# Kernel tuning notes

Measured on AMD Instinct MI355X. Metric: run time of the kernel, lower is better.

The kernel has to match this reference:

```python
import jax, jax.numpy as jnp
import numpy as np
from math import factorial, sqrt

MUL = 128
LS = (0, 1, 2)
NODE_DIM = MUL * (1 + 3 + 5)   # 1152
N_NODES = 10000
N_EDGES = 50000
EDGE_DIM = 20

# ---------- real Wigner-3j (Clebsch-Gordan) coefficients ----------

def _su2_cg(j1, j2, j3, m1, m2, m3):
    if m1 + m2 != m3:
        return 0.0
    f = lambda n: factorial(int(n))
    pref = sqrt((2 * j3 + 1) * f(j1 + j2 - j3) * f(j1 - j2 + j3) * f(-j1 + j2 + j3) / f(j1 + j2 + j3 + 1))
    pref *= sqrt(f(j3 + m3) * f(j3 - m3) * f(j1 - m1) * f(j1 + m1) * f(j2 - m2) * f(j2 + m2))
    s = 0.0
    for k in range(int(j1 + j2 - j3) + 1):
        if min(j1 - m1 - k, j2 + m2 - k, j3 - j2 + m1 + k, j3 - j1 - m2 + k) < 0:
            continue
        s += (-1) ** k / (f(k) * f(j1 + j2 - j3 - k) * f(j1 - m1 - k) * f(j2 + m2 - k) * f(j3 - j2 + m1 + k) * f(j3 - j1 - m2 + k))
    return pref * s

def _q_real_to_complex(l):
    q = np.zeros((2 * l + 1, 2 * l + 1), dtype=np.complex128)
    for m in range(-l, 0):
        q[l + m, l - m] = 1 / np.sqrt(2)
        q[l + m, l + m] = -1j / np.sqrt(2)
    q[l, l] = 1.0
    for m in range(1, l + 1):
        q[l + m, l + m] = (-1) ** m / np.sqrt(2)
        q[l + m, l - m] = 1j * (-1) ** m / np.sqrt(2)
    return (-1j) ** l * q

def _real_w3j(l1, l2, l3):
    C = np.zeros((2 * l1 + 1, 2 * l2 + 1, 2 * l3 + 1))
    for a in range(2 * l1 + 1):
        for b in range(2 * l2 + 1):
            for c in range(2 * l3 + 1):
                C[a, b, c] = _su2_cg(l1, l2, l3, a - l1, b - l2, c - l3)
    Q1, Q2, Q3 = _q_real_to_complex(l1), _q_real_to_complex(l2), _q_real_to_complex(l3)
    T = np.einsum('abc,ai,bj,ck->ijk', C.astype(np.complex128), Q1, Q2, np.conj(Q3))
    W = T.real if np.linalg.norm(T.real) >= np.linalg.norm(T.imag) else T.imag
    return jnp.asarray(W / np.linalg.norm(W), dtype=jnp.float32)

# instructions from get_feasible_tp(irreps_in, irreps_in, irreps_hidden, 'uuu')
TP_PATHS = [(0, 0, 0), (0, 1, 1), (0, 2, 2), (1, 0, 1), (1, 1, 0), (1, 1, 2),
            (1, 2, 1), (2, 0, 2), (2, 1, 1), (2, 2, 0), (2, 2, 2)]
W3J = {p: _real_w3j(*p) for p in set(TP_PATHS)}
N_PATHS_TO = {0: 3, 1: 4, 2: 4}
PW = {l: float(np.sqrt((2 * l + 1) / N_PATHS_TO[l])) for l in LS}  # e3nn component/element norm
WEIGHT_NUMEL = len(TP_PATHS) * MUL  # 1408

# ---------- irreps helpers (e3nn layout: per-irrep [mul, 2l+1] blocks) ----------

def split_irreps(x):
    n = x.shape[0]
    s = x[:, :MUL]
    v1 = x[:, MUL:4 * MUL].reshape(n, MUL, 3)
    v2 = x[:, 4 * MUL:].reshape(n, MUL, 5)
    return s, v1, v2

def merge_irreps(s, v1, v2):
    n = s.shape[0]
    return jnp.concatenate([s, v1.reshape(n, -1), v2.reshape(n, -1)], axis=-1)

def o3_linear(x, W0, W1, W2, b0=None):
    s, v1, v2 = split_irreps(x)
    inv = 1.0 / np.sqrt(MUL)  # e3nn fan-in normalization
    s = s @ W0 * inv + (b0 if b0 is not None else 0.0)
    v1 = jnp.einsum('num,uv->nvm', v1, W1) * inv
    v2 = jnp.einsum('num,uv->nvm', v2, W2) * inv
    return merge_irreps(s, v1, v2)

def norm_gate(x, W1, b1, W2, b2):
    s, v1, v2 = split_irreps(x)
    n1 = jnp.linalg.norm(v1, axis=-1)  # [N, 128]
    n2 = jnp.linalg.norm(v2, axis=-1)
    f0 = jnp.concatenate([s, n1, n2], axis=-1)  # [N, 384]
    g = jax.nn.silu(f0 @ W1 + b1) @ W2 + b2
    return merge_irreps(g[:, :MUL], v1 * g[:, MUL:2 * MUL, None], v2 * g[:, 2 * MUL:, None])

def equiv_dot(x1, x2):
    s1, v11, v21 = split_irreps(x1)
    s2, v12, v22 = split_irreps(x2)
    d0 = s1 * s2
    d1 = jnp.sum(v11 * v12, -1) / np.sqrt(3.0)
    d2 = jnp.sum(v21 * v22, -1) / np.sqrt(5.0)
    return jnp.concatenate([d0, d1, d2], -1)  # [E, 384]

def tp_node_pair(x1, x2, weights):
    s1, v11, v21 = split_irreps(x1)
    s2, v12, v22 = split_irreps(x2)
    parts1 = [s1[:, :, None], v11, v21]
    parts2 = [s2[:, :, None], v12, v22]
    outs = {l: 0.0 for l in LS}
    for p, (l1, l2, l3) in enumerate(TP_PATHS):
        w = weights[:, p * MUL:(p + 1) * MUL]  # [E, 128]
        outs[l3] = outs[l3] + PW[l3] * jnp.einsum(
            'eui,euj,ijk,eu->euk', parts1[l1], parts2[l2], W3J[(l1, l2, l3)], w)
    return merge_irreps(outs[0][:, :, 0], outs[1], outs[2])

# ---------- inputs ----------

def setup_inputs() -> dict:
    key = jax.random.key(0)
    ks = jax.random.split(key, 30)
    lin = lambda k, fi, fo: jax.random.normal(k, (fi, fo), jnp.float32) / np.sqrt(fi)
    vec = lambda k, d: jax.random.normal(k, (d,), jnp.float32) * 0.1
    NI = 3 * MUL  # 384 = num_irreps
    return {
        'x': jax.random.normal(ks[0], (N_NODES, NODE_DIM), jnp.float32),
        'edge_attr': jax.random.uniform(ks[1], (N_EDGES, EDGE_DIM), jnp.float32),
        'edge_index': jax.random.randint(ks[2], (2, N_EDGES), 0, N_NODES, jnp.int32),
        'W_pre0': jax.random.normal(ks[3], (MUL, MUL), jnp.float32),
        'W_pre1': jax.random.normal(ks[4], (MUL, MUL), jnp.float32),
        'W_pre2': jax.random.normal(ks[5], (MUL, MUL), jnp.float32),
        'b_pre0': vec(ks[6], MUL),
        'ngpre_W1': lin(ks[7], NI, NI), 'ngpre_b1': vec(ks[8], NI),
        'ngpre_W2': lin(ks[9], NI, NI), 'ngpre_b2': vec(ks[10], NI),
        'es_W1': lin(ks[11], MUL + NI, 128), 'es_b1': vec(ks[12], 128),
        'es_W2': lin(ks[13], 128, WEIGHT_NUMEL), 'es_b2': vec(ks[14], WEIGHT_NUMEL),
        'er_W1': lin(ks[15], EDGE_DIM, 128), 'er_b1': vec(ks[16], 128),
        'er_W2': lin(ks[17], 128, WEIGHT_NUMEL), 'er_b2': vec(ks[18], WEIGHT_NUMEL),
        'ngpost_W1': lin(ks[19], NI, NI), 'ngpost_b1': vec(ks[20], NI),
        'ngpost_W2': lin(ks[21], NI, NI), 'ngpost_b2': vec(ks[22], NI),
        'W_post0': jax.random.normal(ks[23], (MUL, MUL), jnp.float32),
        'W_post1': jax.random.normal(ks[24], (MUL, MUL), jnp.float32),
        'W_post2': jax.random.normal(ks[25], (MUL, MUL), jnp.float32),
    }

def reference(x, edge_attr, edge_index,
              W_pre0, W_pre1, W_pre2, b_pre0,
              ngpre_W1, ngpre_b1, ngpre_W2, ngpre_b2,
              es_W1, es_b1, es_W2, es_b2,
              er_W1, er_b1, er_W2, er_b2,
              ngpost_W1, ngpost_b1, ngpost_W2, ngpost_b2,
              W_post0, W_post1, W_post2):
    src, dst = edge_index[0], edge_index[1]
    xs, xd = x[src], x[dst]
    dots = equiv_dot(xs, xd)[:, MUL:]  # drop 0e dots: [E, 256]
    s0 = jnp.concatenate([xs[:, :MUL], xd[:, :MUL], dots], axis=-1)  # [E, 512]
    tp_w = (jax.nn.silu(s0 @ es_W1 + es_b1) @ es_W2 + es_b2) \
         * (jax.nn.silu(edge_attr @ er_W1 + er_b1) @ er_W2 + er_b2)  # [E, 1408]
    x_prime = norm_gate(o3_linear(x, W_pre0, W_pre1, W_pre2, b_pre0),
                        ngpre_W1, ngpre_b1, ngpre_W2, ngpre_b2)
    fij = tp_node_pair(x_prime[src], x_prime[dst], tp_w)  # [E, 1152]
    fij = norm_gate(fij, ngpost_W1, ngpost_b1, ngpost_W2, ngpost_b2)
    fij = o3_linear(fij, W_post0, W_post1, W_post2)
    return fij
```

## Files before the change

kernel.cpp:

```cpp
#include <hip/hip_runtime.h>
#include <math.h>

#define NNODES 10000
#define NEDGES 50000
#define ND 1152
#define MUL 128
#define WNW 1408
#define EDIM 20

#define CK1 0.5773502691896258f
#define CK2 0.4472135954999579f
#define A2C 0.31622776601683794f
#define A0A (-0.18257418583505536f)
#define A0B 0.3651483716701107f
#define B1C 0.11952286093343936f
#define B2C 0.23904572186687873f
#define B3C 0.20701966780270626f
#define PW0 0.5773502691896258f
#define PW1 0.8660254037844386f
#define PW2 1.1180339887498949f
#define INV128 0.08838834764831845f

__device__ __forceinline__ float silu_f(float v) { return v / (1.f + expf(-v)); }

typedef short bfrag __attribute__((ext_vector_type(8)));
typedef float f32x4 __attribute__((ext_vector_type(4)));

__device__ __forceinline__ ushort f2bf(float f) {
    uint u = __float_as_uint(f);
    u += 0x7fffu + ((u >> 16) & 1u);
    return (ushort)(u >> 16);
}
__device__ __forceinline__ float bf2f(ushort h) {
    return __uint_as_float(((uint)h) << 16);
}

#define LSTR 40

template<bool DUAL, bool SILU>
__global__ __launch_bounds__(256) void gemmbf(
    const float* __restrict__ A1, int lda,
    const ushort* __restrict__ B1H, const ushort* __restrict__ B1L,
    const float* __restrict__ b1,
    const float* __restrict__ A2,
    const ushort* __restrict__ B2H, const ushort* __restrict__ B2L,
    const float* __restrict__ b2,
    float* __restrict__ C, int ldc, int M, int K)
{
    __shared__ __align__(16) ushort Ah[128 * LSTR];
    __shared__ __align__(16) ushort Al[128 * LSTR];
    __shared__ __align__(16) ushort Bh[128 * LSTR];
    __shared__ __align__(16) ushort Bl[128 * LSTR];

    const int tid = threadIdx.x;
    const int l   = tid & 63;
    const int wid = tid >> 6;
    const int wr  = (wid >> 1) << 6;
    const int wc  = (wid & 1) << 6;
    const int rowBase = blockIdx.y << 7;
    const int n0      = blockIdx.x << 7;

    const int sRow = tid >> 1;
    const int sK   = (tid & 1) << 4;
    const int bN   = tid & 127;
    const int bK   = (tid >> 7) << 4;

    const int frow = l & 15;
    const int fk   = (l >> 4) << 3;

    f32x4 acc0[4][4], acc1[4][4];
#pragma unroll
    for (int m = 0; m < 4; ++m)
#pragma unroll
        for (int n = 0; n < 4; ++n) {
            acc0[m][n] = f32x4{0.f, 0.f, 0.f, 0.f};
            if constexpr (DUAL) acc1[m][n] = f32x4{0.f, 0.f, 0.f, 0.f};
        }

#pragma unroll
    for (int ph = 0; ph < (DUAL ? 2 : 1); ++ph) {
        const float*  A  = (DUAL && ph) ? A2  : A1;
        const ushort* BH = (DUAL && ph) ? B2H : B1H;
        const ushort* BL = (DUAL && ph) ? B2L : B1L;
        for (int k0 = 0; k0 < K; k0 += 32) {
            float f[16];
            int grow = rowBase + sRow;
            if (grow < M) {
                const float4* p = (const float4*)&A[(size_t)grow * lda + k0 + sK];
#pragma unroll
                for (int j = 0; j < 4; ++j) {
                    float4 v = p[j];
                    f[j * 4 + 0] = v.x; f[j * 4 + 1] = v.y;
                    f[j * 4 + 2] = v.z; f[j * 4 + 3] = v.w;
                }
            } else {
#pragma unroll
                for (int j = 0; j < 16; ++j) f[j] = 0.f;
            }
            {
                int base = sRow * LSTR + sK;
#pragma unroll
                for (int j = 0; j < 4; ++j) {
                    ushort4 hv, lv;
                    hv.x = f2bf(f[j * 4 + 0]); lv.x = f2bf(f[j * 4 + 0] - bf2f(hv.x));
                    hv.y = f2bf(f[j * 4 + 1]); lv.y = f2bf(f[j * 4 + 1] - bf2f(hv.y));
                    hv.z = f2bf(f[j * 4 + 2]); lv.z = f2bf(f[j * 4 + 2] - bf2f(hv.z));
                    hv.w = f2bf(f[j * 4 + 3]); lv.w = f2bf(f[j * 4 + 3] - bf2f(hv.w));
                    *(ushort4*)&Ah[base + j * 4] = hv;
                    *(ushort4*)&Al[base + j * 4] = lv;
                }
            }
            {
                size_t go = (size_t)(n0 + bN) * K + k0 + bK;
                uint4 h0 = *(const uint4*)&BH[go];
                uint4 h1 = *(const uint4*)&BH[go + 8];
                uint4 l0 = *(const uint4*)&BL[go];
                uint4 l1 = *(const uint4*)&BL[go + 8];
                int bb = bN * LSTR + bK;
                *(uint4*)&Bh[bb]     = h0;
                *(uint4*)&Bh[bb + 8] = h1;
                *(uint4*)&Bl[bb]     = l0;
                *(uint4*)&Bl[bb + 8] = l1;
            }
            __syncthreads();
            bfrag bhF[4], blF[4];
#pragma unroll
            for (int n = 0; n < 4; ++n) {
                int r = (wc + n * 16 + frow) * LSTR + fk;
                bhF[n] = *(const bfrag*)&Bh[r];
                blF[n] = *(const bfrag*)&Bl[r];
            }
#pragma unroll
            for (int m = 0; m < 4; ++m) {
                int r = (wr + m * 16 + frow) * LSTR + fk;
                bfrag ah = *(const bfrag*)&Ah[r];
                bfrag al = *(const bfrag*)&Al[r];
#pragma unroll
                for (int n = 0; n < 4; ++n) {
                    f32x4 a = (DUAL && ph) ? acc1[m][n] : acc0[m][n];
                    a = __builtin_amdgcn_mfma_f32_16x16x32_bf16(ah, bhF[n], a, 0, 0, 0);
                    a = __builtin_amdgcn_mfma_f32_16x16x32_bf16(ah, blF[n], a, 0, 0, 0);
                    a = __builtin_amdgcn_mfma_f32_16x16x32_bf16(al, bhF[n], a, 0, 0, 0);
                    if (DUAL && ph) acc1[m][n] = a; else acc0[m][n] = a;
                }
            }
            __syncthreads();
        }
    }

#pragma unroll
    for (int n = 0; n < 4; ++n) {
        int col = n0 + wc + n * 16 + frow;
        float bb1 = b1[col];
        float bb2 = DUAL ? b2[col] : 0.f;
#pragma unroll
        for (int m = 0; m < 4; ++m) {
            int row0 = rowBase + wr + m * 16 + ((l >> 4) << 2);
#pragma unroll
            for (int q = 0; q < 4; ++q) {
                int row = row0 + q;
                if (row >= M) continue;
                float v;
                if constexpr (DUAL) {
                    v = (acc0[m][n][q] + bb1) * (acc1[m][n][q] + bb2);
                } else {
                    v = acc0[m][n][q] + bb1;
                    if constexpr (SILU) v = silu_f(v);
                }
                C[(size_t)row * ldc + col] = v;
            }
        }
    }
}

template<int NPL, int OFF, int GOFF>
__global__ __launch_bounds__(256) void o3postbf(
    const float* __restrict__ fij, size_t FP,
    const float* __restrict__ g,
    const ushort* __restrict__ WH, const ushort* __restrict__ WL,
    float* __restrict__ out, int M)
{
    __shared__ __align__(16) ushort Ah[NPL * 32 * LSTR];
    __shared__ __align__(16) ushort Al[NPL * 32 * LSTR];
    __shared__ __align__(16) ushort Bh[128 * LSTR];
// ... 84 lines not shown
    for (int n = 0; n < 4; ++n) {
        int col = wc + n * 16 + frow;
#pragma unroll
        for (int q = 0; q < 4; ++q) {
            int row = rowBase + wr + ((l >> 4) << 2) + q;
            if (row >= M) continue;
            float* po = &out[(size_t)row * ND + OFF + col * NPL];
#pragma unroll
            for (int p = 0; p < NPL; ++p)
                po[p] = acc[p][n][q] * INV128;
        }
    }
}

__global__ void wsplit_kernel(
    const float* __restrict__ W0, const float* __restrict__ W1,
    const float* __restrict__ W2, const float* __restrict__ W3,
    const float* __restrict__ W4, const float* __restrict__ W5,
    const float* __restrict__ W6, const float* __restrict__ W7,
    const float* __restrict__ W8,
    ushort* __restrict__ out)
{
    int m = blockIdx.y;
    const float* W; int K, N; size_t off;
    switch (m) {
        case 0:  W = W0; K = 128; N = 1408; off = 0;        break;
        case 1:  W = W1; K = 128; N = 1408; off = 360448;   break;
        case 2:  W = W2; K = 384; N = 384;  off = 720896;   break;
        case 3:  W = W3; K = 384; N = 384;  off = 1015808;  break;
        case 4:  W = W4; K = 384; N = 384;  off = 1310720;  break;
        case 5:  W = W5; K = 384; N = 384;  off = 1605632;  break;
        case 6:  W = W6; K = 128; N = 128;  off = 1900544;  break;
        case 7:  W = W7; K = 128; N = 128;  off = 1933312;  break;
        default: W = W8; K = 128; N = 128;  off = 1966080;  break;
    }
    int idx = blockIdx.x * 256 + threadIdx.x;
    if (idx >= K * N) return;
    int k = idx / N, n = idx - k * N;
    float v = W[idx];
    ushort h  = f2bf(v);
    ushort lo = f2bf(v - bf2f(h));
    size_t KN = (size_t)K * N;
    out[off + (size_t)n * K + k]      = h;
    out[off + KN + (size_t)n * K + k] = lo;
}

template<int AMODE, int OMODE, bool SILU, bool FMUL, bool O3S>
__global__ __launch_bounds__(256) void gemm128(
    const float* __restrict__ A, int lda,
    const float* __restrict__ B, int ldb,
    const float* __restrict__ W1p, const float* __restrict__ W2p,
    const float* __restrict__ bias, const float* __restrict__ M2,
    float* __restrict__ C, int ldc, int M, int K,
    const float* __restrict__ xg, const int* __restrict__ ei,
    const float* __restrict__ dots)
{
    __shared__ float Ast[32][132];
    __shared__ float Bs[32][132];

    const int tid = threadIdx.x;
    const int tx = tid & 15, ty = tid >> 4;
    const int rowBase = blockIdx.y << 7;
    const int n0 = blockIdx.x << 7;
    const int z = blockIdx.z;

    int off = 0, stride = 1;
    if constexpr (AMODE == 2 || AMODE == 3 || AMODE == 4 || OMODE == 1 || O3S) {
        if (z == 0)      { off = 0;             stride = 1; }
        else if (z < 4)  { off = 128 + (z - 1); stride = 3; }
        else             { off = 512 + (z - 4); stride = 5; }
    }
    const float* Bz = B;
    if constexpr (AMODE >= 2) {
        if (z >= 1 && z < 4) Bz = W1p;
        else if (z >= 4)     Bz = W2p;
    }
    const float* Ab = A;
    if constexpr (AMODE == 3 || AMODE == 4) Ab = A + (size_t)z * M * lda;
    float* Cb = C;
    if constexpr (OMODE == 2) Cb = C + (size_t)z * M * ldc;

    float acc[2][2][4][4] = {};

    for (int k0 = 0; k0 < K; k0 += 32) {
#pragma unroll
        for (int i = 0; i < 4; ++i) {
            int f4 = tid + (i << 8);
            int row = f4 >> 3;
            int kq  = (f4 & 7) << 2;
            int grow = rowBase + row, gk = k0 + kq;
            float4 v = make_float4(0.f, 0.f, 0.f, 0.f);
            if (grow < M) {
                if constexpr (AMODE == 0 || AMODE == 3) {
                    if (gk + 4 <= K) {
                        v = *(const float4*)&Ab[(size_t)grow * lda + gk];
                    } else {
                        float t[4] = {0.f, 0.f, 0.f, 0.f};
#pragma unroll
                        for (int j = 0; j < 4; ++j)
                            if (gk + j < K) t[j] = Ab[(size_t)grow * lda + gk + j];
                        v = make_float4(t[0], t[1], t[2], t[3]);
                    }
                } else if constexpr (AMODE == 1) {
                    if (gk < 128)
                        v = *(const float4*)&xg[(size_t)ei[grow] * ND + gk];
                    else if (gk < 256)
                        v = *(const float4*)&xg[(size_t)ei[NEDGES + grow] * ND + (gk - 128)];
                    else
                        v = *(const float4*)&dots[(size_t)grow * 256 + (gk - 256)];
                } else if constexpr (AMODE == 2) {
                    const float* p = &Ab[(size_t)grow * ND + off];
                    v.x = p[(gk + 0) * stride];
                    v.y = p[(gk + 1) * stride];
                    v.z = p[(gk + 2) * stride];
                    v.w = p[(gk + 3) * stride];
                } else {
                    int gsel = (z == 0) ? 0 : (z < 4 ? 128 : 256);
                    float4 vg = *(const float4*)&xg[(size_t)grow * 384 + gsel + gk];
                    if (z == 0) {
                        v = vg;
                    } else {
                        float4 vf = *(const float4*)&Ab[(size_t)grow * lda + gk];
                        v = make_float4(vf.x * vg.x, vf.y * vg.y,
                                        vf.z * vg.z, vf.w * vg.w);
                    }
                }
            }
            Ast[kq + 0][row] = v.x;
            Ast[kq + 1][row] = v.y;
            Ast[kq + 2][row] = v.z;
            Ast[kq + 3][row] = v.w;
        }
#pragma unroll
        for (int i = 0; i < 4; ++i) {
            int f4 = tid + (i << 8);
            int bk = f4 >> 5;
            int nq = (f4 & 31) << 2;
            float4 v = make_float4(0.f, 0.f, 0.f, 0.f);
            if (k0 + bk < K)
                v = *(const float4*)&Bz[(size_t)(k0 + bk) * ldb + n0 + nq];
            *(float4*)&Bs[bk][nq] = v;
        }
        __syncthreads();
#pragma unroll
        for (int kk = 0; kk < 32; ++kk) {
            float4 a0 = *(const float4*)&Ast[kk][(ty << 2)];
            float4 a1 = *(const float4*)&Ast[kk][64 + (ty << 2)];
            float4 b0 = *(const float4*)&Bs[kk][(tx << 2)];
            float4 b1 = *(const float4*)&Bs[kk][64 + (tx << 2)];
            float ar[2][4] = {{a0.x, a0.y, a0.z, a0.w}, {a1.x, a1.y, a1.z, a1.w}};
            float br[2][4] = {{b0.x, b0.y, b0.z, b0.w}, {b1.x, b1.y, b1.z, b1.w}};
#pragma unroll
            for (int h = 0; h < 2; ++h)
#pragma unroll
                for (int g = 0; g < 2; ++g)
#pragma unroll
                    for (int ii = 0; ii < 4; ++ii)
#pragma unroll
                        for (int jj = 0; jj < 4; ++jj)
                            acc[h][g][ii][jj] = fmaf(ar[h][ii], br[g][jj], acc[h][g][ii][jj]);
        }
        __syncthreads();
    }

#pragma unroll
    for (int h = 0; h < 2; ++h) {
#pragma unroll
        for (int ii = 0; ii < 4; ++ii) {
            int row = rowBase + (h << 6) + (ty << 2) + ii;
            if (row >= M) continue;
#pragma unroll
            for (int g = 0; g < 2; ++g) {
                int colq = n0 + (g << 6) + (tx << 2);
                float o[4];
#pragma unroll
                for (int jj = 0; jj < 4; ++jj) {
                    float v = acc[h][g][ii][jj];
                    int col = colq + jj;
                    if constexpr (O3S) {
                        v *= INV128;
                        if (bias && z == 0) v += bias[col];
                    } else {
                        if (bias) v += bias[col];
                    }
                    if constexpr (SILU) v = silu_f(v);
                    if constexpr (FMUL) v *= M2[(size_t)row * ldc + col];
                    o[jj] = v;
                }
                if constexpr (OMODE == 1) {
                    float* p = &Cb[(size_t)row * ND + off];
#pragma unroll
                    for (int jj = 0; jj < 4; ++jj) p[(colq + jj) * stride] = o[jj];
                } else {
                    *(float4*)&Cb[(size_t)row * ldc + colq] =
                        make_float4(o[0], o[1], o[2], o[3]);
                }
            }
        }
    }
}

__global__ void dots_kernel(const float* __restrict__ x, const int* __restrict__ ei,
                            float* __restrict__ dots)
{
    int idx = blockIdx.x * 256 + threadIdx.x;
    int e = idx >> 8, t = idx & 255;
    if (e >= NEDGES) return;
    const float* ps = x + (size_t)ei[e] * ND;
    const float* pd = x + (size_t)ei[NEDGES + e] * ND;
    float v;
    if (t < 128) {
        int u = 128 + t * 3;
        v = (ps[u] * pd[u] + ps[u + 1] * pd[u + 1] + ps[u + 2] * pd[u + 2]) * CK1;
    } else {
        int u = 512 + (t - 128) * 5;
        v = (ps[u] * pd[u] + ps[u + 1] * pd[u + 1] + ps[u + 2] * pd[u + 2]
             + ps[u + 3] * pd[u + 3] + ps[u + 4] * pd[u + 4]) * CK2;
    }
    dots[idx] = v;
}

__global__ void f0_kernel(const float* __restrict__ in, float* __restrict__ f0, int M)
{
    int idx = blockIdx.x * 256 + threadIdx.x;
    int r = idx / 384, t = idx - r * 384;
    if (r >= M) return;
    size_t P = (size_t)M * 128;
    const float* p = in + (size_t)r * 128;
    float v;
    if (t < 128) v = p[t];
    else if (t < 256) {
        int u = t - 128;
        float x1 = p[P + u], x2 = p[2 * P + u], x3 = p[3 * P + u];
        v = sqrtf(x1 * x1 + x2 * x2 + x3 * x3);
    } else {
        int u = t - 256;
        float x1 = p[4 * P + u], x2 = p[5 * P + u], x3 = p[6 * P + u],
              x4 = p[7 * P + u], x5 = p[8 * P + u];
        v = sqrtf(x1 * x1 + x2 * x2 + x3 * x3 + x4 * x4 + x5 * x5);
    }
    f0[(size_t)r * 384 + t] = v;
}

__global__ void gate_kernel(float* __restrict__ xp, const float* __restrict__ g, int M)
{
    int t = blockIdx.x * 256 + threadIdx.x;
    if (t >= M * 128) return;
    int z = blockIdx.y;
    int r = t >> 7, u = t & 127;
    float* p = xp + (size_t)z * M * 128 + t;
    const float* gr = g + (size_t)r * 384;
    if (z == 0)      *p = gr[u];
    else if (z < 4)  *p *= gr[128 + u];
    else             *p *= gr[256 + u];
}

__global__ __launch_bounds__(256) void tp_kernel(
    const float* __restrict__ xp, const int* __restrict__ ei,
    const float* __restrict__ tpw, float* __restrict__ fij,
    float* __restrict__ f0, int e0, int ec)
{
    int le = blockIdx.x * 2 + (threadIdx.x >> 7);
    int u = threadIdx.x & 127;
    if (le >= ec) return;
    int e = e0 + le;
    const size_t NP = (size_t)NNODES * 128;
    const float* ps = xp + (size_t)ei[e] * 128 + u;
    const float* pd = xp + (size_t)ei[NEDGES + e] * 128 + u;

    float ss = ps[0], sd = pd[0];
    float a0 = ps[NP],     a1 = ps[2 * NP], a2 = ps[3 * NP];
    float b0 = pd[NP],     b1 = pd[2 * NP], b2 = pd[3 * NP];
    float c0 = ps[4 * NP], c1 = ps[5 * NP], c2 = ps[6 * NP],
          c3 = ps[7 * NP], c4 = ps[8 * NP];
    float d0 = pd[4 * NP], d1 = pd[5 * NP], d2 = pd[6 * NP],
// ... 35 lines not shown
    float o2_1 = PW2 * (CK2 * (w2 * ss * d1 + w7 * c1 * sd) + w5 * S1 + w10 * V1);
    float o2_2 = PW2 * (CK2 * (w2 * ss * d2 + w7 * c2 * sd) + w5 * S2 + w10 * V2);
    float o2_3 = PW2 * (CK2 * (w2 * ss * d3 + w7 * c3 * sd) + w5 * S3 + w10 * V3);
    float o2_4 = PW2 * (CK2 * (w2 * ss * d4 + w7 * c4 * sd) + w5 * S4 + w10 * V4);

    size_t FP = (size_t)ec * 128;
    float* po = fij + (size_t)le * 128 + u;
    po[0] = o_s;
    po[FP] = o1_0;     po[2 * FP] = o1_1; po[3 * FP] = o1_2;
    po[4 * FP] = o2_0; po[5 * FP] = o2_1; po[6 * FP] = o2_2;
    po[7 * FP] = o2_3; po[8 * FP] = o2_4;

    float n1 = sqrtf(o1_0 * o1_0 + o1_1 * o1_1 + o1_2 * o1_2);
    float n2 = sqrtf(o2_0 * o2_0 + o2_1 * o2_1 + o2_2 * o2_2
                     + o2_3 * o2_3 + o2_4 * o2_4);
    float* pf = f0 + (size_t)le * 384;
    pf[u] = o_s;
    pf[128 + u] = n1;
    pf[256 + u] = n2;
}

extern "C" void kernel_launch(void* const* d_in, const int* in_sizes, int n_in,
                              void* d_out, int out_size, void* d_ws, size_t ws_size,
                              hipStream_t stream)
{
    const float* x         = (const float*)d_in[0];
    const float* edge_attr = (const float*)d_in[1];
    const int*   ei        = (const int*)  d_in[2];
    const float* W_pre0    = (const float*)d_in[3];
    const float* W_pre1    = (const float*)d_in[4];
    const float* W_pre2    = (const float*)d_in[5];
    const float* b_pre0    = (const float*)d_in[6];
    const float* ngpre_W1  = (const float*)d_in[7];
    const float* ngpre_b1  = (const float*)d_in[8];
// ... 6 lines not shown
    const float* er_W1     = (const float*)d_in[15];
    const float* er_b1     = (const float*)d_in[16];
    const float* er_W2     = (const float*)d_in[17];
    const float* er_b2     = (const float*)d_in[18];
    const float* ngpost_W1 = (const float*)d_in[19];
    const float* ngpost_b1 = (const float*)d_in[20];
    const float* ngpost_W2 = (const float*)d_in[21];
    const float* ngpost_b2 = (const float*)d_in[22];
    const float* W_post0   = (const float*)d_in[23];
    const float* W_post1   = (const float*)d_in[24];
    const float* W_post2   = (const float*)d_in[25];
    float* out = (float*)d_out;
    float* ws  = (float*)d_ws;

    float* xp    = ws;
    float* hes   = ws + (size_t)9 * NNODES * 128;
    float* her   = hes + (size_t)NEDGES * 128;
    ushort* wsp  = (ushort*)(her + (size_t)NEDGES * 128);
    const ushort* esW2tH   = wsp;
    const ushort* esW2tL   = wsp + 180224;
    const ushort* erW2tH   = wsp + 360448;
    const ushort* erW2tL   = wsp + 540672;
    const ushort* preW1H   = wsp + 720896;
    const ushort* preW1L   = wsp + 868352;
    const ushort* preW2H   = wsp + 1015808;
    const ushort* preW2L   = wsp + 1163264;
    const ushort* postW1H  = wsp + 1310720;
    const ushort* postW1L  = wsp + 1458176;
    const ushort* postW2H  = wsp + 1605632;
    const ushort* postW2L  = wsp + 1753088;
    const ushort* o3pW0H   = wsp + 1900544;
    const ushort* o3pW0L   = wsp + 1916928;
    const ushort* o3pW1H   = wsp + 1933312;
    const ushort* o3pW1L   = wsp + 1949696;
    const ushort* o3pW2H   = wsp + 1966080;
    const ushort* o3pW2L   = wsp + 1982464;
    float* arena = her + (size_t)NEDGES * 128 + 999424;

    long ws_floats = (long)(ws_size / 4);
    long arena_f = ws_floats - 25319424L;
    long ec0 = arena_f / 2944;
    if (ec0 > NEDGES) ec0 = NEDGES;
    if (ec0 < 1) ec0 = 1;
    int NC = (int)((NEDGES + ec0 - 1) / ec0);
    int Ec = (NEDGES + NC - 1) / NC;

    float* dots = arena;

    wsplit_kernel<<<dim3(704, 9), 256, 0, stream>>>(
        es_W2, er_W2, ngpre_W1, ngpre_W2, ngpost_W1, ngpost_W2,
        W_post0, W_post1, W_post2, wsp);

    dots_kernel<<<NEDGES, 256, 0, stream>>>(x, ei, dots);

    dim3 gE(1, (NEDGES + 127) / 128);
    gemm128<1, 0, true, false, false><<<gE, 256, 0, stream>>>(
        nullptr, 0, es_W1, 128, nullptr, nullptr, es_b1, nullptr,
        hes, 128, NEDGES, 512, x, ei, dots);
    gemm128<0, 0, true, false, false><<<gE, 256, 0, stream>>>(
        edge_attr, EDIM, er_W1, 128, nullptr, nullptr, er_b1, nullptr,
        her, 128, NEDGES, EDIM, nullptr, nullptr, nullptr);

    dim3 gO3p(1, (NNODES + 127) / 128, 9);
    gemm128<2, 2, false, false, true><<<gO3p, 256, 0, stream>>>(
        x, 0, W_pre0, 128, W_pre1, W_pre2, b_pre0, nullptr,
        xp, 128, NNODES, 128, nullptr, nullptr, nullptr);

    float* f0n = arena;
    float* hb  = f0n + (size_t)NNODES * 384;
    float* gb  = hb + (size_t)NNODES * 384;
    f0_kernel<<<((size_t)NNODES * 384 + 255) / 256, 256, 0, stream>>>(xp, f0n, NNODES);
    dim3 gNGp(3, (NNODES + 127) / 128);
    gemmbf<false, true><<<gNGp, 256, 0, stream>>>(
        f0n, 384, preW1H, preW1L, ngpre_b1,
        nullptr, nullptr, nullptr, nullptr,
        hb, 384, NNODES, 384);
    gemmbf<false, false><<<gNGp, 256, 0, stream>>>(
        hb, 384, preW2H, preW2L, ngpre_b2,
        nullptr, nullptr, nullptr, nullptr,
        gb, 384, NNODES, 384);
    dim3 gGp((NNODES * 128 + 255) / 256, 9);
    gate_kernel<<<gGp, 256, 0, stream>>>(xp, gb, NNODES);

    for (int c = 0; c < NC; ++c) {
        int e0 = c * Ec;
        int ec = NEDGES - e0; if (ec > Ec) ec = Ec;
        if (ec <= 0) break;

        float* tpwc = arena;
        float* fijc = tpwc + (size_t)Ec * 1408;
        float* f0p  = fijc + (size_t)Ec * 1152;

        dim3 gW(11, (ec + 127) / 128);
        gemmbf<true, false><<<gW, 256, 0, stream>>>(
            hes + (size_t)e0 * 128, 128, esW2tH, esW2tL, es_b2,
            her + (size_t)e0 * 128, erW2tH, erW2tL, er_b2,
            tpwc, WNW, ec, 128);

        tp_kernel<<<(ec + 1) / 2, 256, 0, stream>>>(xp, ei, tpwc, fijc, f0p, e0, ec);

        float* h1p = tpwc;
        float* gp  = tpwc + (size_t)Ec * 384;
        dim3 gNG(3, (ec + 127) / 128);
        gemmbf<false, true><<<gNG, 256, 0, stream>>>(
            f0p, 384, postW1H, postW1L, ngpost_b1,
            nullptr, nullptr, nullptr, nullptr,
            h1p, 384, ec, 384);
        gemmbf<false, false><<<gNG, 256, 0, stream>>>(
            h1p, 384, postW2H, postW2L, ngpost_b2,
            nullptr, nullptr, nullptr, nullptr,
            gp, 384, ec, 384);

        size_t FPc = (size_t)ec * 128;
        int nb = (ec + 31) / 32;
        o3postbf<1, 0, 0><<<nb, 256, 0, stream>>>(
            nullptr, 0, gp, o3pW0H, o3pW0L, out + (size_t)e0 * ND, ec);
        o3postbf<3, 128, 128><<<nb, 256, 0, stream>>>(
            fijc + FPc, FPc, gp, o3pW1H, o3pW1L, out + (size_t)e0 * ND, ec);
        o3postbf<5, 512, 256><<<nb, 256, 0, stream>>>(
            fijc + 4 * FPc, FPc, gp, o3pW2H, o3pW2L, out + (size_t)e0 * ND, ec);
    }
}
```

Baseline: 1.414 ms.

## Move remaining fp32 GEMMs to split-bf16 MFMA and store intermediates pre-split

The scalar fp32 gemm128 kernel is replaced by the split-bf16 MFMA gemmbf kernel for the edge-MLP first layers and the pre o3_linear, using new gather and strided input modes. Intermediate activations (hes, her, f0, hidden layers) are now written as hi/lo bf16 pairs, so consumers load them directly instead of converting fp32 in every tile. The aim is to replace FMA-bound scalar GEMMs with matrix-core work and to halve intermediate traffic. The cost is more template variants, element-wise strided or unvectorized loads in the edge_attr and o3 paths, and a changed workspace layout.

```diff
diff --git a/kernel.cpp b/kernel.cpp
--- a/kernel.cpp
+++ b/kernel.cpp
@@ -37,15 +37,19 @@
 
 #define LSTR 40
 
-template<bool DUAL, bool SILU>
+template<int DUAL, int SILU, int ASRC, int OSINK>
 __global__ __launch_bounds__(256) void gemmbf(
-    const float* __restrict__ A1, int lda,
+    const void* __restrict__ A1p, const void* __restrict__ A1s, int lda,
     const ushort* __restrict__ B1H, const ushort* __restrict__ B1L,
     const float* __restrict__ b1,
-    const float* __restrict__ A2,
+    const void* __restrict__ A2p, const void* __restrict__ A2s,
     const ushort* __restrict__ B2H, const ushort* __restrict__ B2L,
     const float* __restrict__ b2,
-    float* __restrict__ C, int ldc, int M, int K)
+    const ushort* __restrict__ W2H, const ushort* __restrict__ W2L,
+    float* __restrict__ C, ushort* __restrict__ CH, ushort* __restrict__ CL,
+    int ldc, int M, int K, int Kreal,
+    const float* __restrict__ xg, const int* __restrict__ ei,
+    const float* __restrict__ dots)
 {
     __shared__ __align__(16) ushort Ah[128 * LSTR];
     __shared__ __align__(16) ushort Al[128 * LSTR];
@@ -68,6 +72,14 @@
     const int frow = l & 15;
     const int fk   = (l >> 4) << 3;
 
+    const int z = (ASRC == 3) ? blockIdx.z : 0;
+    int zoff = 0, zstride = 1;
+    if constexpr (ASRC == 3) {
+        if (z == 0)      { zoff = 0;             zstride = 1; }
+        else if (z < 4)  { zoff = 128 + (z - 1); zstride = 3; }
+        else             { zoff = 512 + (z - 4); zstride = 5; }
+    }
+
     f32x4 acc0[4][4], acc1[4][4];
 #pragma unroll
     for (int m = 0; m < 4; ++m)
@@ -79,48 +91,89 @@
 
 #pragma unroll
     for (int ph = 0; ph < (DUAL ? 2 : 1); ++ph) {
-        const float*  A  = (DUAL && ph) ? A2  : A1;
+        const void* Ap  = (DUAL && ph) ? A2p : A1p;
+        const void* Asp = (DUAL && ph) ? A2s : A1s;
         const ushort* BH = (DUAL && ph) ? B2H : B1H;
         const ushort* BL = (DUAL && ph) ? B2L : B1L;
+        if constexpr (ASRC == 3) {
+            if (z >= 1 && z < 4) { BH = B2H; BL = B2L; }
+            else if (z >= 4)     { BH = W2H; BL = W2L; }
+        }
+
         for (int k0 = 0; k0 < K; k0 += 32) {
-            float f[16];
-            int grow = rowBase + sRow;
-            if (grow < M) {
-                const float4* p = (const float4*)&A[(size_t)grow * lda + k0 + sK];
-#pragma unroll
-                for (int j = 0; j < 4; ++j) {
-                    float4 v = p[j];
-                    f[j * 4 + 0] = v.x; f[j * 4 + 1] = v.y;
-                    f[j * 4 + 2] = v.z; f[j * 4 + 3] = v.w;
-                }
-            } else {
-#pragma unroll
-                for (int j = 0; j < 16; ++j) f[j] = 0.f;
-            }
             {
-                int base = sRow * LSTR + sK;
-#pragma unroll
-                for (int j = 0; j < 4; ++j) {
-                    ushort4 hv, lv;
-                    hv.x = f2bf(f[j * 4 + 0]); lv.x = f2bf(f[j * 4 + 0] - bf2f(hv.x));
-                    hv.y = f2bf(f[j * 4 + 1]); lv.y = f2bf(f[j * 4 + 1] - bf2f(hv.y));
-                    hv.z = f2bf(f[j * 4 + 2]); lv.z = f2bf(f[j * 4 + 2] - bf2f(hv.z));
-                    hv.w = f2bf(f[j * 4 + 3]); lv.w = f2bf(f[j * 4 + 3] - bf2f(hv.w));
-                    *(ushort4*)&Ah[base + j * 4] = hv;
-                    *(ushort4*)&Al[base + j * 4] = lv;
+                int grow = rowBase + sRow;
+                if constexpr (ASRC == 1) {
+                    uint4 h0 = {0,0,0,0}, h1v = {0,0,0,0};
+                    uint4 l0 = {0,0,0,0}, l1v = {0,0,0,0};
+                    if (grow < M) {
+                        const ushort* AH = ((const ushort*)Ap)  + (size_t)grow * lda + k0 + sK;
+                        const ushort* AL = ((const ushort*)Asp) + (size_t)grow * lda + k0 + sK;
+                        h0  = *(const uint4*)AH; h1v = *(const uint4*)(AH + 8);
+                        l0  = *(const uint4*)AL; l1v = *(const uint4*)(AL + 8);
+                    }
+                    int base = sRow * LSTR + sK;
+                    *(uint4*)&Ah[base]     = h0;  *(uint4*)&Ah[base + 8] = h1v;
+                    *(uint4*)&Al[base]     = l0;  *(uint4*)&Al[base + 8] = l1v;
+                } else {
+                    float f[16];
+                    if (grow < M) {
+                        if constexpr (ASRC == 0) {
+#pragma unroll
+                            for (int j = 0; j < 16; ++j) {
+                                int gk = k0 + sK + j;
+                                f[j] = (gk < Kreal)
+                                     ? ((const float*)Ap)[(size_t)grow * lda + gk] : 0.f;
+                            }
+                        } else if constexpr (ASRC == 2) {
+                            int gk = k0 + sK;
+                            const float4* p;
+                            if (gk < 128)
+                                p = (const float4*)&xg[(size_t)ei[grow] * ND + gk];
+                            else if (gk < 256)
+                                p = (const float4*)&xg[(size_t)ei[NEDGES + grow] * ND + (gk - 128)];
+                            else
+                                p = (const float4*)&dots[(size_t)grow * 256 + (gk - 256)];
+#pragma unroll
+                            for (int j = 0; j < 4; ++j) {
+                                float4 v = p[j];
+                                f[j*4+0] = v.x; f[j*4+1] = v.y;
+                                f[j*4+2] = v.z; f[j*4+3] = v.w;
+                            }
+                        } else {
+                            const float* p = &((const float*)Ap)[(size_t)grow * lda + zoff];
+#pragma unroll
+                            for (int j = 0; j < 16; ++j)
+                                f[j] = p[(k0 + sK + j) * zstride];
+                        }
+                    } else {
+#pragma unroll
+                        for (int j = 0; j < 16; ++j) f[j] = 0.f;
+                    }
+                    int base = sRow * LSTR + sK;
+#pragma unroll
+                    for (int j = 0; j < 4; ++j) {
+                        ushort4 hv, lv;
+                        hv.x = f2bf(f[j*4+0]); lv.x = f2bf(f[j*4+0] - bf2f(hv.x));
+                        hv.y = f2bf(f[j*4+1]); lv.y = f2bf(f[j*4+1] - bf2f(hv.y));
+                        hv.z = f2bf(f[j*4+2]); lv.z = f2bf(f[j*4+2] - bf2f(hv.z));
+                        hv.w = f2bf(f[j*4+3]); lv.w = f2bf(f[j*4+3] - bf2f(hv.w));
+                        *(ushort4*)&Ah[base + j*4] = hv;
+                        *(ushort4*)&Al[base + j*4] = lv;
+                    }
                 }
             }
             {
                 size_t go = (size_t)(n0 + bN) * K + k0 + bK;
                 uint4 h0 = *(const uint4*)&BH[go];
-                uint4 h1 = *(const uint4*)&BH[go + 8];
+                uint4 h1v = *(const uint4*)&BH[go + 8];
                 uint4 l0 = *(const uint4*)&BL[go];
-                uint4 l1 = *(const uint4*)&BL[go + 8];
+                uint4 l1v = *(const uint4*)&BL[go + 8];
                 int bb = bN * LSTR + bK;
                 *(uint4*)&Bh[bb]     = h0;
-                *(uint4*)&Bh[bb + 8] = h1;
+                *(uint4*)&Bh[bb + 8] = h1v;
                 *(uint4*)&Bl[bb]     = l0;
-                *(uint4*)&Bl[bb + 8] = l1;
+                *(uint4*)&Bl[bb + 8] = l1v;
             }
             __syncthreads();
             bfrag bhF[4], blF[4];
@@ -151,8 +204,8 @@
 #pragma unroll
     for (int n = 0; n < 4; ++n) {
         int col = n0 + wc + n * 16 + frow;
-        float bb1 = b1[col];
-        float bb2 = DUAL ? b2[col] : 0.f;
+        float bb1 = b1 ? b1[col] : 0.f;
+        float bb2 = (DUAL && b2) ? b2[col] : 0.f;
 #pragma unroll
         for (int m = 0; m < 4; ++m) {
             int row0 = rowBase + wr + m * 16 + ((l >> 4) << 2);
@@ -160,14 +213,25 @@
             for (int q = 0; q < 4; ++q) {
                 int row = row0 + q;
                 if (row >= M) continue;
-                float v;
                 if constexpr (DUAL) {
-                    v = (acc0[m][n][q] + bb1) * (acc1[m][n][q] + bb2);
+                    float v = (acc0[m][n][q] + bb1) * (acc1[m][n][q] + bb2);
+                    C[(size_t)row * ldc + col] = v;
+                } else if constexpr (OSINK == 0) {
+                    float v = acc0[m][n][q] + bb1;
+                    if constexpr (SILU) v = silu_f(v);
+                    C[(size_t)row * ldc + col] = v;
+                } else if constexpr (OSINK == 1) {
+                    float v = acc0[m][n][q] + bb1;
+                    if constexpr (SILU) v = silu_f(v);
+                    ushort h  = f2bf(v);
+                    ushort lo = f2bf(v - bf2f(h));
+                    CH[(size_t)row * ldc + col] = h;
+                    CL[(size_t)row * ldc + col] = lo;
                 } else {
-                    v = acc0[m][n][q] + bb1;
-                    if constexpr (SILU) v = silu_f(v);
+                    float v = acc0[m][n][q] * INV128;
+                    if (z == 0 && b1) v += b1[col];
+                    C[(size_t)z * M * ldc + (size_t)row * ldc + col] = v;
                 }
-                C[(size_t)row * ldc + col] = v;
             }
         }
     }
@@ -282,190 +346,42 @@
 }
 
 __global__ void wsplit_kernel(
-    const float* __restrict__ W0, const float* __restrict__ W1,
-    const float* __restrict__ W2, const float* __restrict__ W3,
-    const float* __restrict__ W4, const float* __restrict__ W5,
-    const float* __restrict__ W6, const float* __restrict__ W7,
-    const float* __restrict__ W8,
+    const float* __restrict__ W0,  const float* __restrict__ W1,
+    const float* __restrict__ W2,  const float* __restrict__ W3,
+    const float* __restrict__ W4,  const float* __restrict__ W5,
+    const float* __restrict__ W6,  const float* __restrict__ W7,
+    const float* __restrict__ W8,  const float* __restrict__ W9,
+    const float* __restrict__ W10, const float* __restrict__ W11,
+    const float* __restrict__ W12, const float* __restrict__ W13,
     ushort* __restrict__ out)
 {
     int m = blockIdx.y;
-    const float* W; int K, N; size_t off;
+    const float* W; int K, Kp, N; size_t off;
     switch (m) {
-        case 0:  W = W0; K = 128; N = 1408; off = 0;        break;
-        case 1:  W = W1; K = 128; N = 1408; off = 360448;   break;
-        case 2:  W = W2; K = 384; N = 384;  off = 720896;   break;
-        case 3:  W = W3; K = 384; N = 384;  off = 1015808;  break;
-        case 4:  W = W4; K = 384; N = 384;  off = 1310720;  break;
-        case 5:  W = W5; K = 384; N = 384;  off = 1605632;  break;
-        case 6:  W = W6; K = 128; N = 128;  off = 1900544;  break;
-        case 7:  W = W7; K = 128; N = 128;  off = 1933312;  break;
-        default: W = W8; K = 128; N = 128;  off = 1966080;  break;
+        case 0:  W = W0;  K = 128; Kp = 128; N = 1408; off = 0;       break;
+        case 1:  W = W1;  K = 128; Kp = 128; N = 1408; off = 360448;  break;
+        case 2:  W = W2;  K = 384; Kp = 384; N = 384;  off = 720896;  break;
+        case 3:  W = W3;  K = 384; Kp = 384; N = 384;  off = 1015808; break;
+        case 4:  W = W4;  K = 384; Kp = 384; N = 384;  off = 1310720; break;
+        case 5:  W = W5;  K = 384; Kp = 384; N = 384;  off = 1605632; break;
+        case 6:  W = W6;  K = 128; Kp = 128; N = 128;  off = 1900544; break;
+        case 7:  W = W7;  K = 128; Kp = 128; N = 128;  off = 1933312; break;
+        case 8:  W = W8;  K = 128; Kp = 128; N = 128;  off = 1966080; break;
+        case 9:  W = W9;  K = 128; Kp = 128; N = 128;  off = 1998848; break;
+        case 10: W = W10; K = 128; Kp = 128; N = 128;  off = 2031616; break;
+        case 11: W = W11; K = 128; Kp = 128; N = 128;  off = 2064384; break;
+        case 12: W = W12; K = 512; Kp = 512; N = 128;  off = 2097152; break;
+        default: W = W13; K = 20;  Kp = 32;  N = 128;  off = 2228224; break;
     }
     int idx = blockIdx.x * 256 + threadIdx.x;
-    if (idx >= K * N) return;
+    if (idx >= Kp * N) return;
     int k = idx / N, n = idx - k * N;
-    float v = W[idx];
+    float v = (k < K) ? W[(size_t)k * N + n] : 0.f;
     ushort h  = f2bf(v);
     ushort lo = f2bf(v - bf2f(h));
-    size_t KN = (size_t)K * N;
-    out[off + (size_t)n * K + k]      = h;
-    out[off + KN + (size_t)n * K + k] = lo;
-}
-
-template<int AMODE, int OMODE, bool SILU, bool FMUL, bool O3S>
-__global__ __launch_bounds__(256) void gemm128(
-    const float* __restrict__ A, int lda,
-    const float* __restrict__ B, int ldb,
-    const float* __restrict__ W1p, const float* __restrict__ W2p,
-    const float* __restrict__ bias, const float* __restrict__ M2,
-    float* __restrict__ C, int ldc, int M, int K,
-    const float* __restrict__ xg, const int* __restrict__ ei,
-    const float* __restrict__ dots)
-{
-    __shared__ float Ast[32][132];
-    __shared__ float Bs[32][132];
-
-    const int tid = threadIdx.x;
-    const int tx = tid & 15, ty = tid >> 4;
-    const int rowBase = blockIdx.y << 7;
-    const int n0 = blockIdx.x << 7;
-    const int z = blockIdx.z;
-
-    int off = 0, stride = 1;
-    if constexpr (AMODE == 2 || AMODE == 3 || AMODE == 4 || OMODE == 1 || O3S) {
-        if (z == 0)      { off = 0;             stride = 1; }
-        else if (z < 4)  { off = 128 + (z - 1); stride = 3; }
-        else             { off = 512 + (z - 4); stride = 5; }
-    }
-    const float* Bz = B;
-    if constexpr (AMODE >= 2) {
-        if (z >= 1 && z < 4) Bz = W1p;
-        else if (z >= 4)     Bz = W2p;
-    }
-    const float* Ab = A;
-    if constexpr (AMODE == 3 || AMODE == 4) Ab = A + (size_t)z * M * lda;
-    float* Cb = C;
-    if constexpr (OMODE == 2) Cb = C + (size_t)z * M * ldc;
-
-    float acc[2][2][4][4] = {};
-
-    for (int k0 = 0; k0 < K; k0 += 32) {
-#pragma unroll
-        for (int i = 0; i < 4; ++i) {
-            int f4 = tid + (i << 8);
-            int row = f4 >> 3;
-            int kq  = (f4 & 7) << 2;
-            int grow = rowBase + row, gk = k0 + kq;
-            float4 v = make_float4(0.f, 0.f, 0.f, 0.f);
-            if (grow < M) {
-                if constexpr (AMODE == 0 || AMODE == 3) {
-                    if (gk + 4 <= K) {
-                        v = *(const float4*)&Ab[(size_t)grow * lda + gk];
-                    } else {
-                        float t[4] = {0.f, 0.f, 0.f, 0.f};
-#pragma unroll
-                        for (int j = 0; j < 4; ++j)
-                            if (gk + j < K) t[j] = Ab[(size_t)grow * lda + gk + j];
-                        v = make_float4(t[0], t[1], t[2], t[3]);
-                    }
-                } else if constexpr (AMODE == 1) {
-                    if (gk < 128)
-                        v = *(const float4*)&xg[(size_t)ei[grow] * ND + gk];
-                    else if (gk < 256)
-                        v = *(const float4*)&xg[(size_t)ei[NEDGES + grow] * ND + (gk - 128)];
-                    else
-                        v = *(const float4*)&dots[(size_t)grow * 256 + (gk - 256)];
-                } else if constexpr (AMODE == 2) {
-                    const float* p = &Ab[(size_t)grow * ND + off];
-                    v.x = p[(gk + 0) * stride];
-                    v.y = p[(gk + 1) * stride];
-                    v.z = p[(gk + 2) * stride];
-                    v.w = p[(gk + 3) * stride];
-                } else {
-                    int gsel = (z == 0) ? 0 : (z < 4 ? 128 : 256);
-                    float4 vg = *(const float4*)&xg[(size_t)grow * 384 + gsel + gk];
-                    if (z == 0) {
-                        v = vg;
-                    } else {
-                        float4 vf = *(const float4*)&Ab[(size_t)grow * lda + gk];
-                        v = make_float4(vf.x * vg.x, vf.y * vg.y,
-                                        vf.z * vg.z, vf.w * vg.w);
-                    }
-                }
-            }
-            Ast[kq + 0][row] = v.x;
-            Ast[kq + 1][row] = v.y;
-            Ast[kq + 2][row] = v.z;
-            Ast[kq + 3][row] = v.w;
-        }
-#pragma unroll
-        for (int i = 0; i < 4; ++i) {
-            int f4 = tid + (i << 8);
-            int bk = f4 >> 5;
-            int nq = (f4 & 31) << 2;
-            float4 v = make_float4(0.f, 0.f, 0.f, 0.f);
-            if (k0 + bk < K)
-                v = *(const float4*)&Bz[(size_t)(k0 + bk) * ldb + n0 + nq];
-            *(float4*)&Bs[bk][nq] = v;
-        }
-        __syncthreads();
-#pragma unroll
-        for (int kk = 0; kk < 32; ++kk) {
-            float4 a0 = *(const float4*)&Ast[kk][(ty << 2)];
-            float4 a1 = *(const float4*)&Ast[kk][64 + (ty << 2)];
-            float4 b0 = *(const float4*)&Bs[kk][(tx << 2)];
-            float4 b1 = *(const float4*)&Bs[kk][64 + (tx << 2)];
-            float ar[2][4] = {{a0.x, a0.y, a0.z, a0.w}, {a1.x, a1.y, a1.z, a1.w}};
-            float br[2][4] = {{b0.x, b0.y, b0.z, b0.w}, {b1.x, b1.y, b1.z, b1.w}};
-#pragma unroll
-            for (int h = 0; h < 2; ++h)
-#pragma unroll
-                for (int g = 0; g < 2; ++g)
-#pragma unroll
-                    for (int ii = 0; ii < 4; ++ii)
-#pragma unroll
-                        for (int jj = 0; jj < 4; ++jj)
-                            acc[h][g][ii][jj] = fmaf(ar[h][ii], br[g][jj], acc[h][g][ii][jj]);
-        }
-        __syncthreads();
-    }
-
-#pragma unroll
-    for (int h = 0; h < 2; ++h) {
-#pragma unroll
-        for (int ii = 0; ii < 4; ++ii) {
-            int row = rowBase + (h << 6) + (ty << 2) + ii;
-            if (row >= M) continue;
-#pragma unroll
-            for (int g = 0; g < 2; ++g) {
-                int colq = n0 + (g << 6) + (tx << 2);
-                float o[4];
-#pragma unroll
-                for (int jj = 0; jj < 4; ++jj) {
-                    float v = acc[h][g][ii][jj];
-                    int col = colq + jj;
-                    if constexpr (O3S) {
-                        v *= INV128;
-                        if (bias && z == 0) v += bias[col];
-                    } else {
-                        if (bias) v += bias[col];
-                    }
-                    if constexpr (SILU) v = silu_f(v);
-                    if constexpr (FMUL) v *= M2[(size_t)row * ldc + col];
-                    o[jj] = v;
-                }
-                if constexpr (OMODE == 1) {
-                    float* p = &Cb[(size_t)row * ND + off];
-#pragma unroll
-                    for (int jj = 0; jj < 4; ++jj) p[(colq + jj) * stride] = o[jj];
-                } else {
-                    *(float4*)&Cb[(size_t)row * ldc + colq] =
-                        make_float4(o[0], o[1], o[2], o[3]);
-                }
-            }
-        }
-    }
+    size_t KN = (size_t)Kp * N;
+    out[off + (size_t)n * Kp + k]      = h;
+    out[off + KN + (size_t)n * Kp + k] = lo;
 }
 
 __global__ void dots_kernel(const float* __restrict__ x, const int* __restrict__ ei,
@@ -488,7 +404,8 @@
     dots[idx] = v;
 }
 
-__global__ void f0_kernel(const float* __restrict__ in, float* __restrict__ f0, int M)
+__global__ void f0_kernel(const float* __restrict__ in,
+                          ushort* __restrict__ f0H, ushort* __restrict__ f0L, int M)
 {
     int idx = blockIdx.x * 256 + threadIdx.x;
     int r = idx / 384, t = idx - r * 384;
@@ -507,7 +424,9 @@
               x4 = p[7 * P + u], x5 = p[8 * P + u];
         v = sqrtf(x1 * x1 + x2 * x2 + x3 * x3 + x4 * x4 + x5 * x5);
     }
-    f0[(size_t)r * 384 + t] = v;
+    ushort h = f2bf(v);
+    f0H[(size_t)r * 384 + t] = h;
+    f0L[(size_t)r * 384 + t] = f2bf(v - bf2f(h));
 }
 
 __global__ void gate_kernel(float* __restrict__ xp, const float* __restrict__ g, int M)
@@ -526,7 +445,7 @@
 __global__ __launch_bounds__(256) void tp_kernel(
     const float* __restrict__ xp, const int* __restrict__ ei,
     const float* __restrict__ tpw, float* __restrict__ fij,
-    float* __restrict__ f0, int e0, int ec)
+    ushort* __restrict__ f0H, ushort* __restrict__ f0L, int e0, int ec)
 {
     int le = blockIdx.x * 2 + (threadIdx.x >> 7);
     int u = threadIdx.x & 127;
@@ -592,10 +511,11 @@
     float n1 = sqrtf(o1_0 * o1_0 + o1_1 * o1_1 + o1_2 * o1_2);
     float n2 = sqrtf(o2_0 * o2_0 + o2_1 * o2_1 + o2_2 * o2_2
                      + o2_3 * o2_3 + o2_4 * o2_4);
-    float* pf = f0 + (size_t)le * 384;
-    pf[u] = o_s;
-    pf[128 + u] = n1;
-    pf[256 + u] = n2;
+    size_t fb = (size_t)le * 384;
+    ushort h;
+    h = f2bf(o_s); f0H[fb + u]       = h; f0L[fb + u]       = f2bf(o_s - bf2f(h));
+    h = f2bf(n1);  f0H[fb + 128 + u] = h; f0L[fb + 128 + u] = f2bf(n1 - bf2f(h));
+    h = f2bf(n2);  f0H[fb + 256 + u] = h; f0L[fb + 256 + u] = f2bf(n2 - bf2f(h));
 }
 
 extern "C" void kernel_launch(void* const* d_in, const int* in_sizes, int n_in,
@@ -632,31 +552,43 @@
     float* ws  = (float*)d_ws;
 
     float* xp    = ws;
-    float* hes   = ws + (size_t)9 * NNODES * 128;
-    float* her   = hes + (size_t)NEDGES * 128;
-    ushort* wsp  = (ushort*)(her + (size_t)NEDGES * 128);
-    const ushort* esW2tH   = wsp;
-    const ushort* esW2tL   = wsp + 180224;
-    const ushort* erW2tH   = wsp + 360448;
-    const ushort* erW2tL   = wsp + 540672;
-    const ushort* preW1H   = wsp + 720896;
-    const ushort* preW1L   = wsp + 868352;
-    const ushort* preW2H   = wsp + 1015808;
-    const ushort* preW2L   = wsp + 1163264;
-    const ushort* postW1H  = wsp + 1310720;
-    const ushort* postW1L  = wsp + 1458176;
-    const ushort* postW2H  = wsp + 1605632;
-    const ushort* postW2L  = wsp + 1753088;
-    const ushort* o3pW0H   = wsp + 1900544;
-    const ushort* o3pW0L   = wsp + 1916928;
-    const ushort* o3pW1H   = wsp + 1933312;
-    const ushort* o3pW1L   = wsp + 1949696;
-    const ushort* o3pW2H   = wsp + 1966080;
-    const ushort* o3pW2L   = wsp + 1982464;
-    float* arena = her + (size_t)NEDGES * 128 + 999424;
+    ushort* hesH = (ushort*)ws + 23040000;
+    ushort* hesL = hesH + 6400000;
+    ushort* herH = hesL + 6400000;
+    ushort* herL = herH + 6400000;
+    ushort* wsp  = herL + 6400000;
+    const ushort* esW2H  = wsp;
+    const ushort* esW2L  = wsp + 180224;
+    const ushort* erW2H  = wsp + 360448;
+    const ushort* erW2L  = wsp + 540672;
+    const ushort* preW1H = wsp + 720896;
+    const ushort* preW1L = wsp + 868352;
+    const ushort* preW2H = wsp + 1015808;
+    const ushort* preW2L = wsp + 1163264;
+    const ushort* postW1H = wsp + 1310720;
+    const ushort* postW1L = wsp + 1458176;
+    const ushort* postW2H = wsp + 1605632;
+    const ushort* postW2L = wsp + 1753088;
+    const ushort* o3pW0H = wsp + 1900544;
+    const ushort* o3pW0L = wsp + 1916928;
+    const ushort* o3pW1H = wsp + 1933312;
+    const ushort* o3pW1L = wsp + 1949696;
+    const ushort* o3pW2H = wsp + 1966080;
+    const ushort* o3pW2L = wsp + 1982464;
+    const ushort* preL0H = wsp + 1998848;
+    const ushort* preL0L = wsp + 2015232;
+    const ushort* preL1H = wsp + 2031616;
+    const ushort* preL1L = wsp + 2048000;
+    const ushort* preL2H = wsp + 2064384;
+    const ushort* preL2L = wsp + 2080768;
+    const ushort* esW1H  = wsp + 2097152;
+    const ushort* esW1L  = wsp + 2162688;
+    const ushort* erW1H  = wsp + 2228224;
+    const ushort* erW1L  = wsp + 2232320;
+    float* arena = ws + 25438208;
 
     long ws_floats = (long)(ws_size / 4);
-    long arena_f = ws_floats - 25319424L;
+    long arena_f = ws_floats - 25438208L;
     long ec0 = arena_f / 2944;
     if (ec0 > NEDGES) ec0 = NEDGES;
     if (ec0 < 1) ec0 = 1;
@@ -665,38 +597,44 @@
 
     float* dots = arena;
 
-    wsplit_kernel<<<dim3(704, 9), 256, 0, stream>>>(
+    wsplit_kernel<<<dim3(704, 14), 256, 0, stream>>>(
         es_W2, er_W2, ngpre_W1, ngpre_W2, ngpost_W1, ngpost_W2,
-        W_post0, W_post1, W_post2, wsp);
+        W_post0, W_post1, W_post2, W_pre0, W_pre1, W_pre2,
+        es_W1, er_W1, wsp);
 
     dots_kernel<<<NEDGES, 256, 0, stream>>>(x, ei, dots);
 
     dim3 gE(1, (NEDGES + 127) / 128);
-    gemm128<1, 0, true, false, false><<<gE, 256, 0, stream>>>(
-        nullptr, 0, es_W1, 128, nullptr, nullptr, es_b1, nullptr,
-        hes, 128, NEDGES, 512, x, ei, dots);
-    gemm128<0, 0, true, false, false><<<gE, 256, 0, stream>>>(
-        edge_attr, EDIM, er_W1, 128, nullptr, nullptr, er_b1, nullptr,
-        her, 128, NEDGES, EDIM, nullptr, nullptr, nullptr);
+    gemmbf<0, 1, 2, 1><<<gE, 256, 0, stream>>>(
+        nullptr, nullptr, 0, esW1H, esW1L, es_b1,
+        nullptr, nullptr, nullptr, nullptr, nullptr, nullptr, nullptr,
+        nullptr, hesH, hesL, 128, NEDGES, 512, 512, x, ei, dots);
+    gemmbf<0, 1, 0, 1><<<gE, 256, 0, stream>>>(
+        edge_attr, nullptr, EDIM, erW1H, erW1L, er_b1,
+        nullptr, nullptr, nullptr, nullptr, nullptr, nullptr, nullptr,
+        nullptr, herH, herL, 128, NEDGES, 32, EDIM, nullptr, nullptr, nullptr);
 
     dim3 gO3p(1, (NNODES + 127) / 128, 9);
-    gemm128<2, 2, false, false, true><<<gO3p, 256, 0, stream>>>(
-        x, 0, W_pre0, 128, W_pre1, W_pre2, b_pre0, nullptr,
-        xp, 128, NNODES, 128, nullptr, nullptr, nullptr);
-
-    float* f0n = arena;
-    float* hb  = f0n + (size_t)NNODES * 384;
-    float* gb  = hb + (size_t)NNODES * 384;
-    f0_kernel<<<((size_t)NNODES * 384 + 255) / 256, 256, 0, stream>>>(xp, f0n, NNODES);
+    gemmbf<0, 0, 3, 2><<<gO3p, 256, 0, stream>>>(
+        x, nullptr, ND, preL0H, preL0L, b_pre0,
+        nullptr, nullptr, preL1H, preL1L, nullptr, preL2H, preL2L,
+        xp, nullptr, nullptr, 128, NNODES, 128, 128, nullptr, nullptr, nullptr);
+
+    ushort* f0nH = (ushort*)arena;
+    ushort* f0nL = f0nH + (size_t)NNODES * 384;
+    ushort* hbH  = f0nL + (size_t)NNODES * 384;
+    ushort* hbL  = hbH + (size_t)NNODES * 384;
+    float*  gb   = arena + (size_t)NNODES * 384 * 2;
+    f0_kernel<<<((size_t)NNODES * 384 + 255) / 256, 256, 0, stream>>>(xp, f0nH, f0nL, NNODES);
     dim3 gNGp(3, (NNODES + 127) / 128);
-    gemmbf<false, true><<<gNGp, 256, 0, stream>>>(
-        f0n, 384, preW1H, preW1L, ngpre_b1,
-        nullptr, nullptr, nullptr, nullptr,
-        hb, 384, NNODES, 384);
-    gemmbf<false, false><<<gNGp, 256, 0, stream>>>(
-        hb, 384, preW2H, preW2L, ngpre_b2,
-        nullptr, nullptr, nullptr, nullptr,
-        gb, 384, NNODES, 384);
+    gemmbf<0, 1, 1, 1><<<gNGp, 256, 0, stream>>>(
+        f0nH, f0nL, 384, preW1H, preW1L, ngpre_b1,
+        nullptr, nullptr, nullptr, nullptr, nullptr, nullptr, nullptr,
+        nullptr, hbH, hbL, 384, NNODES, 384, 384, nullptr, nullptr, nullptr);
+    gemmbf<0, 0, 1, 0><<<gNGp, 256, 0, stream>>>(
+        hbH, hbL, 384, preW2H, preW2L, ngpre_b2,
+        nullptr, nullptr, nullptr, nullptr, nullptr, nullptr, nullptr,
+        gb, nullptr, nullptr, 384, NNODES, 384, 384, nullptr, nullptr, nullptr);
     dim3 gGp((NNODES * 128 + 255) / 256, 9);
     gate_kernel<<<gGp, 256, 0, stream>>>(xp, gb, NNODES);
 
@@ -705,29 +643,33 @@
         int ec = NEDGES - e0; if (ec > Ec) ec = Ec;
         if (ec <= 0) break;
 
-        float* tpwc = arena;
-        float* fijc = tpwc + (size_t)Ec * 1408;
-        float* f0p  = fijc + (size_t)Ec * 1152;
+        float* tpwc  = arena;
+        float* fijc  = tpwc + (size_t)Ec * 1408;
+        ushort* f0pH = (ushort*)(fijc + (size_t)Ec * 1152);
+        ushort* f0pL = f0pH + (size_t)Ec * 384;
 
         dim3 gW(11, (ec + 127) / 128);
-        gemmbf<true, false><<<gW, 256, 0, stream>>>(
-            hes + (size_t)e0 * 128, 128, esW2tH, esW2tL, es_b2,
-            her + (size_t)e0 * 128, erW2tH, erW2tL, er_b2,
-            tpwc, WNW, ec, 128);
-
-        tp_kernel<<<(ec + 1) / 2, 256, 0, stream>>>(xp, ei, tpwc, fijc, f0p, e0, ec);
-
-        float* h1p = tpwc;
-        float* gp  = tpwc + (size_t)Ec * 384;
+        gemmbf<1, 0, 1, 0><<<gW, 256, 0, stream>>>(
+            hesH + (size_t)e0 * 128, hesL + (size_t)e0 * 128, 128,
+            esW2H, esW2L, es_b2,
+            herH + (size_t)e0 * 128, herL + (size_t)e0 * 128,
+            erW2H, erW2L, er_b2, nullptr, nullptr,
+            tpwc, nullptr, nullptr, WNW, ec, 128, 128, nullptr, nullptr, nullptr);
+
+        tp_kernel<<<(ec + 1) / 2, 256, 0, stream>>>(xp, ei, tpwc, fijc, f0pH, f0pL, e0, ec);
+
+        ushort* h1H = (ushort*)tpwc;
+        ushort* h1L = h1H + (size_t)Ec * 384;
+        float*  gp  = tpwc + (size_t)Ec * 384;
         dim3 gNG(3, (ec + 127) / 128);
-        gemmbf<false, true><<<gNG, 256, 0, stream>>>(
-            f0p, 384, postW1H, postW1L, ngpost_b1,
-            nullptr, nullptr, nullptr, nullptr,
-            h1p, 384, ec, 384);
-        gemmbf<false, false><<<gNG, 256, 0, stream>>>(
-            h1p, 384, postW2H, postW2L, ngpost_b2,
-            nullptr, nullptr, nullptr, nullptr,
-            gp, 384, ec, 384);
+        gemmbf<0, 1, 1, 1><<<gNG, 256, 0, stream>>>(
+            f0pH, f0pL, 384, postW1H, postW1L, ngpost_b1,
+            nullptr, nullptr, nullptr, nullptr, nullptr, nullptr, nullptr,
+            nullptr, h1H, h1L, 384, ec, 384, 384, nullptr, nullptr, nullptr);
+        gemmbf<0, 0, 1, 0><<<gNG, 256, 0, stream>>>(
+            h1H, h1L, 384, postW2H, postW2L, ngpost_b2,
+            nullptr, nullptr, nullptr, nullptr, nullptr, nullptr, nullptr,
+            gp, nullptr, nullptr, 384, ec, 384, 384, nullptr, nullptr, nullptr);
 
         size_t FPc = (size_t)ec * 128;
         int nb = (ec + 31) / 32;
```

Result: slower. 1.486 ms (+5.1%).
